# Kernel optimization log

Hardware: AMD Instinct MI355X
Metric: run time of the kernel (lower is better)

## Reference

```python
import jax, jax.numpy as jnp
import numpy as np

B, S, H = 4, 2048, 512
DEPTH, EXP = 2, 4
MAX_LR = 0.1
C = 8            # n_chunks
L = S // C       # chunk length
HE = H * EXP


def _l2norm(x, eps=1e-12):
    n = jnp.sqrt(jnp.sum(x * x, axis=-1, keepdims=True))
    return x / jnp.maximum(n, eps)


def _mem_fwd(mw1, mb1, mw2, mb2, x):
    # ResLinear: residual MLP blocks, x <- x + W2 @ silu(W1 @ x + b1) + b2
    for d in range(DEPTH):
        h = jax.nn.silu(x @ mw1[d].T + mb1[d])
        x = x + h @ mw2[d].T + mb2[d]
    return x


def setup_inputs() -> dict:
    key = jax.random.key(0)
    ks = jax.random.split(key, 9)
    s = 1.0 / np.sqrt(H)
    s2 = 1.0 / np.sqrt(HE)
    return {
        "x": jax.random.normal(ks[0], (B, S, H), jnp.float32),
        "wq": jax.random.normal(ks[1], (H, H), jnp.float32) * s, "bq": jnp.zeros((H,), jnp.float32),
        "wk": jax.random.normal(ks[2], (H, H), jnp.float32) * s, "bk": jnp.zeros((H,), jnp.float32),
        "wv": jax.random.normal(ks[3], (H, H), jnp.float32) * s, "bv": jnp.zeros((H,), jnp.float32),
        "wlr": jax.random.normal(ks[4], (1, H), jnp.float32) * s, "blr": jnp.zeros((1,), jnp.float32),
        "wf": jax.random.normal(ks[5], (1, H), jnp.float32) * s, "bf": jnp.zeros((1,), jnp.float32),
        "wm": jax.random.normal(ks[6], (1, H), jnp.float32) * s, "bm": jnp.zeros((1,), jnp.float32),
        "mw1": jax.random.normal(ks[7], (DEPTH, HE, H), jnp.float32) * s,
        "mb1": jnp.zeros((DEPTH, HE), jnp.float32),
        "mw2": jax.random.normal(ks[8], (DEPTH, H, HE), jnp.float32) * s2,
        "mb2": jnp.zeros((DEPTH, H), jnp.float32),
        "mom_w1": jnp.zeros((DEPTH, HE, H), jnp.float32),
        "mom_b1": jnp.zeros((DEPTH, HE), jnp.float32),
        "mom_w2": jnp.zeros((DEPTH, H, HE), jnp.float32),
        "mom_b2": jnp.zeros((DEPTH, H), jnp.float32),
    }


def reference(x, wq, bq, wk, bk, wv, bv, wlr, blr, wf, bf, wm, bm,
              mw1, mb1, mw2, mb2, mom_w1, mom_b1, mom_w2, mom_b2):
    # projections (non-generating path; S % C == 0 so no padding)
    q = _l2norm(x @ wq.T + bq)                            # [B,S,H]
    k = _l2norm(x @ wk.T + bk).reshape(B, C, L, H)
    v = (x @ wv.T + bv).reshape(B, C, L, H)
    lr = jax.nn.sigmoid(x @ wlr.T + blr).reshape(B, C, L, 1) * MAX_LR
    forget = jax.nn.sigmoid(x @ wf.T + bf).reshape(B, C, L, 1)
    momg = jax.nn.sigmoid(x @ wm.T + bm).reshape(B, C, L, 1)

    mem = (mw1, mb1, mw2, mb2)

    def chunk_loss(mem_params, k_c, v_c, lr_c):
        # k_c,v_c: [B,L,H]; lr_c: [B,L,1]
        preds = _mem_fwd(*mem_params, k_c)
        loss = jnp.mean((preds - v_c) ** 2, axis=-1)      # [B,L]
        return jnp.sum(loss * lr_c[..., 0])

    # per-chunk synthetic gradients of the memory MLP, then mean over chunks
    grads = jax.vmap(jax.grad(chunk_loss), in_axes=(None, 1, 1, 1))(mem, k, v, lr)
    grads = jax.tree_util.tree_map(lambda g: jnp.mean(g, axis=0), grads)

    alpha = jnp.mean(forget, axis=(1, 2, 3))              # [B] forget gate
    theta = jnp.mean(lr, axis=(1, 2, 3))                  # [B] adaptive lr
    eta = jnp.mean(momg, axis=(1, 2, 3))                  # [B] momentum gate

    def update(p, g, m):
        shp = (B,) + (1,) * p.ndim
        a, t, e = alpha.reshape(shp), theta.reshape(shp), eta.reshape(shp)
        m_b = e * m[None] - t * g[None]                   # [B,*p.shape]
        return jnp.mean(p[None] * (1.0 - a) + m_b, axis=0)

    moms = (mom_w1, mom_b1, mom_w2, mom_b2)
    new_mem = tuple(update(p, g, m) for p, g, m in zip(mem, grads, moms))

    return _mem_fwd(*new_mem, q)                          # [B,S,H]
```

## Files before the change

### kernel.cpp

```cpp
#include <hip/hip_runtime.h>
#include <cstdint>
#include <cstddef>


#define NROWS 8192
#define HDIM  512
#define HEDIM 2048
#define NCHUNK 8
#define BK    64
#define DPCOEF (2.0f / (HDIM * NCHUNK))

typedef unsigned short u16;
typedef __attribute__((ext_vector_type(8))) unsigned short u16x8;
typedef __attribute__((ext_vector_type(8))) short bf16x8;
typedef __attribute__((ext_vector_type(4))) float f32x4;

__device__ __forceinline__ float sigmoidf_(float x){ return 1.0f/(1.0f+__expf(-x)); }
__device__ __forceinline__ float siluf_(float x){ return x*sigmoidf_(x); }
__device__ __forceinline__ float dsiluf_(float x){ float s=sigmoidf_(x); return s*(1.0f+x*(1.0f-s)); }
__device__ __forceinline__ u16 bf1_(float x){
    union{float f; unsigned u;} v; v.f = x;
    return (u16)((v.u + 0x7fffu + ((v.u>>16)&1u)) >> 16);
}
__device__ __forceinline__ unsigned bfpack_(float a, float b){
    union{float f; unsigned u;} ua, ub; ua.f = a; ub.f = b;
    unsigned ra = (ua.u + 0x7fffu + ((ua.u>>16)&1u)) >> 16;
    unsigned rb = (ub.u + 0x7fffu + ((ub.u>>16)&1u)) & 0xffff0000u;
    return ra | rb;
}
__device__ __forceinline__ float bf2f_(u16 h){
    union{unsigned u; float f;} v; v.u = ((unsigned)h) << 16; return v.f;
}
__device__ __forceinline__ int swkey_(int row){
    return (((row>>3)&1)<<2) | (((row>>4)&1)<<1) | ((row>>5)&1);
}
__device__ __forceinline__ void gl_lds16(const u16* g, u16* l){
    __builtin_amdgcn_global_load_lds(
        (const __attribute__((address_space(1))) unsigned*)g,
        (__attribute__((address_space(3))) unsigned*)l, 16, 0, 0);
}

template<int MODE, bool ATR>
__global__ __launch_bounds__(256)
void mgemm_k(const u16* __restrict__ A, const u16* __restrict__ B,
             const float* __restrict__ bias, const float* __restrict__ resF,
             const u16* __restrict__ resB, const u16* __restrict__ aux,
             const float* __restrict__ vf, const float* __restrict__ lrs,
             float* __restrict__ outF, u16* __restrict__ outB, u16* __restrict__ outB2,
             int M, int N, int K, int lda, int ldb, int ldv)
{
    __shared__ __align__(128) u16 As[128*64];
    __shared__ __align__(128) u16 Bs[128*64];
    const int tid = threadIdx.x;
    const int lane = tid & 63, wvi = tid >> 6;
    const int wm = wvi >> 1, wn = wvi & 1;
    const int lr = lane & 15, lq = lane >> 4;

    const int gx = gridDim.x;
    const int nwg = gx * gridDim.y;
    int bid = blockIdx.y * gx + blockIdx.x;
    bid = (bid & 7) * (nwg >> 3) + (bid >> 3);
    const int m0 = (bid / gx) * 128, n0 = (bid % gx) * 128;

    int kbeg = 0, kend = K;
    if (MODE == 3){ const int ks = K >> 4; kbeg = blockIdx.z * ks; kend = kbeg + ks; }

    f32x4 acc[4][4];
    const f32x4 zz = {0.f,0.f,0.f,0.f};
    #pragma unroll
    for (int i = 0; i < 4; ++i)
        #pragma unroll
        for (int j = 0; j < 4; ++j) acc[i][j] = zz;

    for (int k0 = kbeg; k0 < kend; k0 += BK) {
        if (!ATR) {
            #pragma unroll
            for (int it = 0; it < 4; ++it){
                const int seg = it*4 + wvi;
                const int key = (((seg&1)<<2)|(((seg>>1)&1)<<1)|((seg>>2)&1));
                const int row = seg*8 + (lane>>3);
                const int chunk = (lane&7) ^ key;
                gl_lds16(A + (size_t)(m0+row)*lda + k0 + chunk*8, &As[seg*512]);
                gl_lds16(B + (size_t)(n0+row)*ldb + k0 + chunk*8, &Bs[seg*512]);
            }
        } else {
            const int mc = tid & 15, kp = tid >> 4;
            const int key = (((mc&1)<<2)|(((mc>>1)&1)<<1)|((mc>>2)&1));
            const int cs = ((kp >> 1) ^ key) * 8 + (kp & 1) * 4;
            {
                const u16* p = A + (size_t)(k0 + 4*kp) * lda + m0 + mc*8;
                u16x8 r0 = *(const u16x8*)p;
                u16x8 r1 = *(const u16x8*)(p + lda);
                u16x8 r2 = *(const u16x8*)(p + 2*lda);
                u16x8 r3 = *(const u16x8*)(p + 3*lda);
                #pragma unroll
                for (int j = 0; j < 8; ++j){
                    uint2 w;
                    w.x = (unsigned)r0[j] | ((unsigned)r1[j] << 16);
                    w.y = (unsigned)r2[j] | ((unsigned)r3[j] << 16);
                    *(uint2*)&As[(mc*8 + j)*64 + cs] = w;
                }
            }
            {
                const u16* p = B + (size_t)(k0 + 4*kp) * ldb + n0 + mc*8;
                u16x8 r0 = *(const u16x8*)p;
                u16x8 r1 = *(const u16x8*)(p + ldb);
                u16x8 r2 = *(const u16x8*)(p + 2*ldb);
                u16x8 r3 = *(const u16x8*)(p + 3*ldb);
                #pragma unroll
                for (int j = 0; j < 8; ++j){
                    uint2 w;
                    w.x = (unsigned)r0[j] | ((unsigned)r1[j] << 16);
                    w.y = (unsigned)r2[j] | ((unsigned)r3[j] << 16);
                    *(uint2*)&Bs[(mc*8 + j)*64 + cs] = w;
                }
            }
        }
        __syncthreads();
        #pragma unroll
        for (int ks = 0; ks < 2; ++ks) {
            bf16x8 afr[4], bfr[4];
            #pragma unroll
            for (int i = 0; i < 4; ++i){
                const int ra = wm*64 + i*16 + lr, rb = wn*64 + i*16 + lr;
                afr[i] = *(const bf16x8*)&As[ra*64 + (((ks*4 + lq) ^ swkey_(ra)) << 3)];
                bfr[i] = *(const bf16x8*)&Bs[rb*64 + (((ks*4 + lq) ^ swkey_(rb)) << 3)];
            }
            #pragma unroll
            for (int mi = 0; mi < 4; ++mi)
                #pragma unroll
                for (int ni = 0; ni < 4; ++ni)
                    acc[mi][ni] = __builtin_amdgcn_mfma_f32_16x16x32_bf16(afr[mi], bfr[ni], acc[mi][ni], 0, 0, 0);
        }
        __syncthreads();
    }

    if (MODE == 3){
        unsigned* P32 = (unsigned*)outB;
        const size_t zb = (size_t)blockIdx.z * ((size_t)M * N / 2);
        #pragma unroll
        for (int ni = 0; ni < 4; ++ni){
            const int col = n0 + wn*64 + ni*16 + lr;
            #pragma unroll
            for (int mi = 0; mi < 4; ++mi){
                const int pr = (m0 + wm*64 + mi*16 + lq*4) >> 1;
                P32[zb + (size_t)pr*N + col]     = bfpack_(acc[mi][ni][0], acc[mi][ni][1]);
                P32[zb + (size_t)(pr+1)*N + col] = bfpack_(acc[mi][ni][2], acc[mi][ni][3]);
            }
        }
        return;
    }

    #pragma unroll
    for (int ni = 0; ni < 4; ++ni){
        const int col = n0 + wn*64 + ni*16 + lr;
        float bv = 0.0f;
        if (MODE==0 || MODE==1 || MODE==2 || MODE==6 || MODE==7 || MODE==8 || MODE==9) bv = bias[col];
        #pragma unroll
        for (int mi = 0; mi < 4; ++mi){
            const int rbase = m0 + wm*64 + mi*16 + lq*4;
            #pragma unroll
            for (int v = 0; v < 4; ++v){
                const int row = rbase + v;
                const size_t idx = (size_t)row * N + col;
                const float o = acc[mi][ni][v];
                if (MODE == 0){ outF[idx] = o + bv; }
                else if (MODE == 1){
                    const float u = o + bv;
                    outB[idx]  = bf1_(siluf_(u));
                    outB2[idx] = bf1_(dsiluf_(u));
                }
                else if (MODE == 2){ outB[idx] = bf1_(siluf_(o + bv)); }
                else if (MODE == 4){ outB[idx] = bf1_(o * bf2f_(aux[idx])); }
                else if (MODE == 5){ outB[idx] = bf1_(o + resF[idx]); }
                else if (MODE == 6){ const float t = o + bv + resF[idx]; outF[idx] = t; outB[idx] = bf1_(t); }
                else if (MODE == 7){ outF[idx] = o + bv + resF[idx]; }
                else if (MODE == 8){
                    const float t = o + bv + bf2f_(resB[idx]);
                    const float g = lrs[row] * DPCOEF * (t - vf[(size_t)row * ldv + col]);
                    outF[idx] = g; outB[idx] = bf1_(g);
                }
                else if (MODE == 9){ outB[idx] = bf1_(o + bv + bf2f_(resB[idx])); }
            }
        }
    }
}

#define XSLOTS   (NROWS*HDIM/8)
#define W1SLOTS  (2*HEDIM*HDIM/8)
#define KVQSLOTS (3*HDIM*HDIM/8)
__global__ __launch_bounds__(256)
void prep_all_k(const float* __restrict__ x,  u16* __restrict__ xb,
                const float* __restrict__ mw1, u16* __restrict__ mw1b,
                const float* __restrict__ mw2, u16* __restrict__ mw2b,
                const float* __restrict__ wk, const float* __restrict__ wv,
                const float* __restrict__ wq, u16* __restrict__ wkvqb,
                const float* __restrict__ bk, const float* __restrict__ bv,
                const float* __restrict__ bq, float* __restrict__ bkvq)
{
    const int id = blockIdx.x * 256 + threadIdx.x;
    const int W1S = 2*HEDIM*HDIM/8;
    const float* src; u16* dst; int i;
    if (id < XSLOTS){ src = x; dst = xb; i = id; }
    else if (id < XSLOTS + W1S){ src = mw1; dst = mw1b; i = id - XSLOTS; }
    else if (id < XSLOTS + 2*W1S){ src = mw2; dst = mw2b; i = id - XSLOTS - W1S; }
    else if (id < XSLOTS + 2*W1S + KVQSLOTS){
        const int j = id - XSLOTS - 2*W1S;
        const int per = HDIM*HDIM/8;
        src = (j < per) ? wk : (j < 2*per ? wv : wq);
        i = (j < per) ? j : (j < 2*per ? j - per : j - 2*per);
        dst = wkvqb + (size_t)(j - i) * 8 * 0 + (size_t)j*8 - (size_t)i*8;
        dst = wkvqb + ((size_t)j - i) * 8;
    }
    else {
        const int j = id - XSLOTS - 2*W1S - KVQSLOTS;
        if (j < 3*HDIM)
            bkvq[j] = (j < HDIM) ? bk[j] : (j < 2*HDIM ? bv[j-HDIM] : bq[j-2*HDIM]);
        return;
    }
    const float4 a = *(const float4*)(src + (size_t)i*8);
    const float4 b = *(const float4*)(src + (size_t)i*8 + 4);
    u16x8 o;
    o[0]=bf1_(a.x); o[1]=bf1_(a.y); o[2]=bf1_(a.z); o[3]=bf1_(a.w);
    o[4]=bf1_(b.x); o[5]=bf1_(b.y); o[6]=bf1_(b.z); o[7]=bf1_(b.w);
    *(u16x8*)(dst + (size_t)i*8) = o;
}

__global__ __launch_bounds__(256)
void tcvt_k(const float* __restrict__ in, u16* __restrict__ out, int R, int C)
{
    __shared__ float t[32][33];
    const int tx = threadIdx.x & 31, ty = threadIdx.x >> 5;
    const int c0 = blockIdx.x * 32, r0 = blockIdx.y * 32;
    #pragma unroll
    for (int j = 0; j < 4; ++j)
        t[ty + 8*j][tx] = in[(size_t)(r0 + ty + 8*j) * C + c0 + tx];
    __syncthreads();
    #pragma unroll
    for (int j = 0; j < 4; ++j)
        out[(size_t)(c0 + ty + 8*j) * R + r0 + tx] = bf1_(t[tx][ty + 8*j]);
}

template<bool WF32>
__global__ __launch_bounds__(64)
void l2norm_k(const float* __restrict__ in, int ld,
              float* __restrict__ outF, u16* __restrict__ outB)
{
    const float* p = in + (size_t)blockIdx.x * ld;
    const int t = threadIdx.x;
    float4 v0 = *(const float4*)(p + t*8), v1 = *(const float4*)(p + t*8 + 4);
    float s = v0.x*v0.x+v0.y*v0.y+v0.z*v0.z+v0.w*v0.w
            + v1.x*v1.x+v1.y*v1.y+v1.z*v1.z+v1.w*v1.w;
    #pragma unroll
    for (int o = 1; o < 64; o <<= 1) s += __shfl_xor(s, o);
    const float sc = 1.0f / fmaxf(sqrtf(s), 1e-12f);
    v0.x*=sc; v0.y*=sc; v0.z*=sc; v0.w*=sc;
    v1.x*=sc; v1.y*=sc; v1.z*=sc; v1.w*=sc;
    if (WF32){
        float* q = outF + (size_t)blockIdx.x * HDIM;
        *(float4*)(q + t*8) = v0; *(float4*)(q + t*8 + 4) = v1;
    }
    u16x8 ob;
    ob[0]=bf1_(v0.x); ob[1]=bf1_(v0.y); ob[2]=bf1_(v0.z); ob[3]=bf1_(v0.w);
    ob[4]=bf1_(v1.x); ob[5]=bf1_(v1.y); ob[6]=bf1_(v1.z); ob[7]=bf1_(v1.w);
    *(u16x8*)(outB + (size_t)blockIdx.x * HDIM + t*8) = ob;
}

__global__ __launch_bounds__(64)
void gates_k(const float* __restrict__ x,
             const float* __restrict__ wlr, const float* __restrict__ blr,
             const float* __restrict__ wf,  const float* __restrict__ bfp,
             const float* __restrict__ wm,  const float* __restrict__ bm,
             float* __restrict__ lr_s, float* __restrict__ f_s, float* __restrict__ m_s)
{
    const size_t row = blockIdx.x;
    const float* p = x + row * HDIM;
    const int t = threadIdx.x;
    float s0 = 0.f, s1 = 0.f, s2 = 0.f;
    #pragma unroll
    for (int i = 0; i < 8; i += 4){
        float4 xv = *(const float4*)(p   + t*8 + i);
        float4 a  = *(const float4*)(wlr + t*8 + i);
        float4 b  = *(const float4*)(wf  + t*8 + i);
        float4 c  = *(const float4*)(wm  + t*8 + i);
        s0 += xv.x*a.x + xv.y*a.y + xv.z*a.z + xv.w*a.w;
        s1 += xv.x*b.x + xv.y*b.y + xv.z*b.z + xv.w*b.w;
        s2 += xv.x*c.x + xv.y*c.y + xv.z*c.z + xv.w*c.w;
    }
    #pragma unroll
    for (int o = 1; o < 64; o <<= 1){
        s0 += __shfl_xor(s0, o); s1 += __shfl_xor(s1, o); s2 += __shfl_xor(s2, o);
    }
    if (t == 0){
        lr_s[row] = sigmoidf_(s0 + blr[0]) * 0.1f;
        f_s[row]  = sigmoidf_(s1 + bfp[0]);
        m_s[row]  = sigmoidf_(s2 + bm[0]);
    }
}

__global__ __launch_bounds__(256)
void scalars_k(const float* __restrict__ lr_s, const float* __restrict__ f_s,
               const float* __restrict__ m_s, float* __restrict__ sc)
{
    __shared__ float sh0[256], sh1[256], sh2[256];
    const int t = threadIdx.x;
    float s0 = 0.f, s1 = 0.f, s2 = 0.f;
    for (int i = t; i < NROWS; i += 256){ s0 += f_s[i]; s1 += lr_s[i]; s2 += m_s[i]; }
    sh0[t] = s0; sh1[t] = s1; sh2[t] = s2;
    __syncthreads();
    for (int o = 128; o > 0; o >>= 1){
        if (t < o){ sh0[t] += sh0[t+o]; sh1[t] += sh1[t+o]; sh2[t] += sh2[t+o]; }
        __syncthreads();
    }
    if (t == 0){
        sc[0] = sh0[0] / (float)NROWS;
        sc[1] = sh1[0] / (float)NROWS;
        sc[2] = sh2[0] / (float)NROWS;
    }
}

template<typename T>
__global__ __launch_bounds__(64)
void colsum_part_k(const T* __restrict__ g, float* __restrict__ part, int cols)
{
    const int c = blockIdx.x * 64 + threadIdx.x;
    const int rc = blockIdx.y;
    const T* p = g + (size_t)rc * 128 * cols + c;
    float s = 0.f;
    for (int r = 0; r < 128; ++r){
        if (sizeof(T) == 2) s += bf2f_(*(const u16*)(p + (size_t)r * cols));
        else                s += *(const float*)(p + (size_t)r * cols);
    }
    part[(size_t)rc * cols + c] = s;
}

__global__ __launch_bounds__(256)
void colsum_upd_k(const float* __restrict__ part, const float* __restrict__ p,
                  const float* __restrict__ mom, const float* __restrict__ sc,
                  float* __restrict__ nb, int cols)
{
    const int c = blockIdx.x * 256 + threadIdx.x;
    if (c < cols){
        float s = 0.f;
        for (int r = 0; r < 64; ++r) s += part[(size_t)r * cols + c];
        nb[c] = p[c] * (1.0f - sc[0]) + sc[2] * mom[c] - sc[1] * s;
    }
}

__global__ __launch_bounds__(256)
void fupdate16p_k(const float* __restrict__ p, const unsigned* __restrict__ P32,
                  const float* __restrict__ mom, const float* __restrict__ sc,
                  u16* __restrict__ nWb, int N, int MN2)
{
    const int i = blockIdx.x * 256 + threadIdx.x;
    if (i < MN2){
        float g0 = 0.f, g1 = 0.f;
        #pragma unroll
        for (int z = 0; z < 16; ++z){
            const unsigned w = P32[(size_t)z * MN2 + i];
            g0 += bf2f_((u16)(w & 0xffffu));
            g1 += bf2f_((u16)(w >> 16));
        }
        const int c = i & (N - 1);
        const size_t r0 = ((size_t)(i / N) * 2) * N + c;
        nWb[r0]     = bf1_(p[r0]     * (1.0f - sc[0]) + sc[2] * mom[r0]     - sc[1] * g0);
        nWb[r0 + N] = bf1_(p[r0 + N] * (1.0f - sc[0]) + sc[2] * mom[r0 + N] - sc[1] * g1);
    }
}

extern "C" void kernel_launch(void* const* d_in, const int* in_sizes, int n_in,
                              void* d_out, int out_size, void* d_ws, size_t ws_size,
                              hipStream_t stream)
{
    const float* x      = (const float*)d_in[0];
    const float* wq     = (const float*)d_in[1];
    const float* bq     = (const float*)d_in[2];
    const float* wk     = (const float*)d_in[3];
    const float* bk     = (const float*)d_in[4];
    const float* wv     = (const float*)d_in[5];
    const float* bv     = (const float*)d_in[6];
    const float* wlr    = (const float*)d_in[7];
    const float* blr    = (const float*)d_in[8];
    const float* wf     = (const float*)d_in[9];
    const float* bfp    = (const float*)d_in[10];
    const float* wm     = (const float*)d_in[11];
    const float* bm     = (const float*)d_in[12];
    const float* mw1    = (const float*)d_in[13];
    const float* mb1    = (const float*)d_in[14];
    const float* mw2    = (const float*)d_in[15];
    const float* mb2    = (const float*)d_in[16];
    const float* mom_w1 = (const float*)d_in[17];
    const float* mom_b1 = (const float*)d_in[18];
    const float* mom_w2 = (const float*)d_in[19];
    const float* mom_b2 = (const float*)d_in[20];
    float* out = (float*)d_out;

    char* base = (char*)d_ws;
    size_t off = 0;
    auto alloc = [&](size_t bytes)->char*{ char* p = base + off; off += (bytes + 255) & ~(size_t)255; return p; };
    const size_t NHf  = (size_t)NROWS * HDIM  * 4;
    const size_t NHb  = (size_t)NROWS * HDIM  * 2;
    const size_t NHEb = (size_t)NROWS * HEDIM * 2;
    const int    WHALF = HEDIM * HDIM;

    float* F2   = (float*)alloc(NHf);
    u16*  xb    = (u16*) alloc(NHb);
    u16*  kb    = (u16*) alloc(NHb);
    u16*  x1b   = (u16*) alloc(NHb);
    u16*  g2b   = (u16*) alloc(NHb);
    u16*  hb    = (u16*) alloc(NHEb);
    u16*  db    = (u16*) alloc(NHEb);
    u16*  dhb   = (u16*) alloc(NHEb + NHf);
    u16*  wkvqb = (u16*) alloc((size_t)3*HDIM*HDIM*2);
    float* bkvq = (float*)alloc((size_t)3*HDIM*4);
    u16*  mw1b  = (u16*) alloc((size_t)2*WHALF*2);
    u16*  mw2b  = (u16*) alloc((size_t)2*WHALF*2);
    u16*  mw2Tb = (u16*) alloc((size_t)2*WHALF*2);
    u16*  mw1T1b= (u16*) alloc((size_t)WHALF*2);
    u16*  nW1b  = (u16*) alloc((size_t)2*WHALF*2);
    u16*  nW2b  = (u16*) alloc((size_t)2*WHALF*2);
    float* cpart= (float*)alloc((size_t)64*HEDIM*4);
    float* lr_s = (float*)alloc((size_t)NROWS*4);
    float* f_s  = (float*)alloc((size_t)NROWS*4);
    float* m_s  = (float*)alloc((size_t)NROWS*4);
    float* sc   = (float*)alloc(64);
    float* nb1  = (float*)alloc((size_t)2*HEDIM*4);
    float* nb2  = (float*)alloc((size_t)2*HDIM*4);
    u16* qb  = xb;
    u16* g1b = g2b;
    float* P3 = (float*)dhb;
    float* F1 = (float*)((char*)dhb + NHEb);
    unsigned* Pp = (unsigned*)db;

    const dim3 blk(256);
    const dim3 gKVQ (3*HDIM/128, NROWS/128);
    const dim3 gN512 (HDIM/128,  NROWS/128);
    const dim3 gN2048(HEDIM/128, NROWS/128);
    const dim3 gTN2  (HEDIM/128, HDIM/128, 16);
    const dim3 gTN1  (HDIM/128,  HEDIM/128, 16);
    const int MN2 = WHALF / 2;

    const float* mw1_1 = mw1 + (size_t)WHALF;
    const float* mw2_1 = mw2 + (size_t)WHALF;

    #define GARG(Ab,Bb,bi,rF,rB,ax,vv,ll,oF,oB,oB2,M,N,K,la,lb,lv) \
        ((const u16*)(Ab),(const u16*)(Bb),(const float*)(bi),(const float*)(rF),\
         (const u16*)(rB),(const u16*)(ax),(const float*)(vv),(const float*)(ll),\
         (float*)(oF),(u16*)(oB),(u16*)(oB2),(M),(N),(K),(la),(lb),(lv))

    {
        const int nblk = (XSLOTS + 2*(2*HEDIM*HDIM/8) + KVQSLOTS)/256 + (3*HDIM + 255)/256;
        prep_all_k<<<dim3(nblk), blk, 0, stream>>>(x, xb, mw1, mw1b, mw2, mw2b,
                                                   wk, wv, wq, wkvqb, bk, bv, bq, bkvq);
    }
    tcvt_k<<<dim3(HEDIM/32, HDIM/32), blk, 0, stream>>>(mw2,   mw2Tb,         HDIM, HEDIM);
    tcvt_k<<<dim3(HEDIM/32, HDIM/32), blk, 0, stream>>>(mw2_1, mw2Tb + WHALF, HDIM, HEDIM);
    tcvt_k<<<dim3(HDIM/32, HEDIM/32), blk, 0, stream>>>(mw1_1, mw1T1b,        HEDIM, HDIM);
    gates_k<<<NROWS, 64, 0, stream>>>(x, wlr, blr, wf, bfp, wm, bm, lr_s, f_s, m_s);
    scalars_k<<<1, blk, 0, stream>>>(lr_s, f_s, m_s, sc);

    mgemm_k<0,false><<<gKVQ, blk, 0, stream>>>GARG(xb, wkvqb, bkvq, 0,0,0,0,0, P3, 0,0, NROWS,3*HDIM,HDIM, HDIM,HDIM, 3*HDIM);
    l2norm_k<false><<<NROWS, 64, 0, stream>>>(P3,          3*HDIM, nullptr, kb);
    l2norm_k<true ><<<NROWS, 64, 0, stream>>>(P3 + 2*HDIM, 3*HDIM, F2, qb);

    mgemm_k<2,false><<<gN2048, blk, 0, stream>>>GARG(kb, mw1b, mb1, 0,0,0,0,0, 0, hb, 0, NROWS,HEDIM,HDIM, HDIM,HDIM, HEDIM);
    mgemm_k<9,false><<<gN512, blk, 0, stream>>>GARG(hb, mw2b, mb2, 0, kb, 0,0,0, 0, x1b, 0, NROWS,HDIM,HEDIM, HEDIM,HEDIM, HDIM);
    mgemm_k<1,false><<<gN2048, blk, 0, stream>>>GARG(x1b, mw1b+WHALF, mb1+HEDIM, 0,0,0,0,0, 0, hb, db, NROWS,HEDIM,HDIM, HDIM,HDIM, HEDIM);
    mgemm_k<8,false><<<gN512, blk, 0, stream>>>GARG(hb, mw2b+WHALF, mb2+HDIM, 0, x1b, 0, P3 + HDIM, lr_s, out, g2b, 0, NROWS,HDIM,HEDIM, HEDIM,HEDIM, 3*HDIM);

    colsum_part_k<float><<<dim3(HDIM/64,64), 64, 0, stream>>>(out, cpart, HDIM);
    colsum_upd_k<<<dim3(HDIM/256), blk, 0, stream>>>(cpart, mb2+HDIM, mom_b2+HDIM, sc, nb2+HDIM, HDIM);
    mgemm_k<4,false><<<gN2048, blk, 0, stream>>>GARG(g2b, mw2Tb+WHALF, 0,0,0, db, 0,0, 0, dhb, 0, NROWS,HEDIM,HDIM, HDIM,HDIM, HEDIM);
    mgemm_k<3,true><<<gTN2, blk, 0, stream>>>GARG(g2b, hb, 0,0,0,0,0,0, 0, Pp, 0, HDIM,HEDIM,NROWS, HDIM,HEDIM, HEDIM);
    fupdate16p_k<<<dim3((MN2+255)/256), blk, 0, stream>>>(mw2_1, Pp, mom_w2+WHALF, sc, nW2b+WHALF, HEDIM, MN2);
    colsum_part_k<u16><<<dim3(HEDIM/64,64), 64, 0, stream>>>(dhb, cpart, HEDIM);
    colsum_upd_k<<<dim3(HEDIM/256), blk, 0, stream>>>(cpart, mb1+HEDIM, mom_b1+HEDIM, sc, nb1+HEDIM, HEDIM);
    mgemm_k<3,true><<<gTN1, blk, 0, stream>>>GARG(dhb, x1b, 0,0,0,0,0,0, 0, Pp, 0, HEDIM,HDIM,NROWS, HEDIM,HDIM, HDIM);
    fupdate16p_k<<<dim3((MN2+255)/256), blk, 0, stream>>>(mw1_1, Pp, mom_w1+WHALF, sc, nW1b+WHALF, HDIM, MN2);
    mgemm_k<5,false><<<gN512, blk, 0, stream>>>GARG(dhb, mw1T1b, 0, out, 0,0,0,0, 0, g1b, 0, NROWS,HDIM,HEDIM, HEDIM,HEDIM, HDIM);

    colsum_part_k<u16><<<dim3(HDIM/64,64), 64, 0, stream>>>(g1b, cpart, HDIM);
    colsum_upd_k<<<dim3(HDIM/256), blk, 0, stream>>>(cpart, mb2, mom_b2, sc, nb2, HDIM);
    mgemm_k<1,false><<<gN2048, blk, 0, stream>>>GARG(kb, mw1b, mb1, 0,0,0,0,0, 0, hb, db, NROWS,HEDIM,HDIM, HDIM,HDIM, HEDIM);
    mgemm_k<4,false><<<gN2048, blk, 0, stream>>>GARG(g1b, mw2Tb, 0,0,0, db, 0,0, 0, dhb, 0, NROWS,HEDIM,HDIM, HDIM,HDIM, HEDIM);
    mgemm_k<3,true><<<gTN2, blk, 0, stream>>>GARG(g1b, hb, 0,0,0,0,0,0, 0, Pp, 0, HDIM,HEDIM,NROWS, HDIM,HEDIM, HEDIM);
    fupdate16p_k<<<dim3((MN2+255)/256), blk, 0, stream>>>(mw2, Pp, mom_w2, sc, nW2b, HEDIM, MN2);
    colsum_part_k<u16><<<dim3(HEDIM/64,64), 64, 0, stream>>>(dhb, cpart, HEDIM);
    colsum_upd_k<<<dim3(HEDIM/256), blk, 0, stream>>>(cpart, mb1, mom_b1, sc, nb1, HEDIM);
    mgemm_k<3,true><<<gTN1, blk, 0, stream>>>GARG(dhb, kb, 0,0,0,0,0,0, 0, Pp, 0, HEDIM,HDIM,NROWS, HEDIM,HDIM, HDIM);
    fupdate16p_k<<<dim3((MN2+255)/256), blk, 0, stream>>>(mw1, Pp, mom_w1, sc, nW1b, HDIM, MN2);

    mgemm_k<2,false><<<gN2048, blk, 0, stream>>>GARG(qb, nW1b, nb1, 0,0,0,0,0, 0, hb, 0, NROWS,HEDIM,HDIM, HDIM,HDIM, HEDIM);
    mgemm_k<6,false><<<gN512, blk, 0, stream>>>GARG(hb, nW2b, nb2, F2, 0,0,0,0, F1, x1b, 0, NROWS,HDIM,HEDIM, HEDIM,HEDIM, HDIM);
    mgemm_k<2,false><<<gN2048, blk, 0, stream>>>GARG(x1b, nW1b+WHALF, nb1+HEDIM, 0,0,0,0,0, 0, hb, 0, NROWS,HEDIM,HDIM, HDIM,HDIM, HEDIM);
    mgemm_k<7,false><<<gN512, blk, 0, stream>>>GARG(hb, nW2b+WHALF, nb2+HDIM, F1, 0,0,0,0, out, 0,0, NROWS,HDIM,HEDIM, HEDIM,HEDIM, HDIM);

    #undef GARG
    (void)in_sizes; (void)n_in; (void)out_size; (void)ws_size;
}
```

Baseline: 807.4 us.

## Double-buffer GEMM K-loop and keep layer-0 activations to skip recompute

The NT GEMM path now stages the next K tile into a second LDS buffer via global_load_lds while the current tile runs MFMA, with explicit vmcnt waits and raw barriers in place of __syncthreads. The TN path prefetches the next tile into registers and writes it to LDS after the current MFMA step. Separately, when the workspace is large enough, the first-layer hidden activation and its silu derivative are saved during the forward pass, so the backward pass no longer recomputes the layer-0 GEMM. This doubles LDS use for NT kernels, which may lower occupancy, and uses more workspace memory.

```diff
diff --git a/kernel.cpp b/kernel.cpp
--- a/kernel.cpp
+++ b/kernel.cpp
@@ -39,6 +39,10 @@
         (const __attribute__((address_space(1))) unsigned*)g,
         (__attribute__((address_space(3))) unsigned*)l, 16, 0, 0);
 }
+__device__ __forceinline__ void bar_(){ asm volatile("s_barrier" ::: "memory"); }
+#define VMCNT8  asm volatile("s_waitcnt vmcnt(8)" ::: "memory")
+#define VMCNT0  asm volatile("s_waitcnt vmcnt(0)" ::: "memory")
+#define LGKM0   asm volatile("s_waitcnt lgkmcnt(0)" ::: "memory")
 
 template<int MODE, bool ATR>
 __global__ __launch_bounds__(256)
@@ -49,8 +53,9 @@
              float* __restrict__ outF, u16* __restrict__ outB, u16* __restrict__ outB2,
              int M, int N, int K, int lda, int ldb, int ldv)
 {
-    __shared__ __align__(128) u16 As[128*64];
-    __shared__ __align__(128) u16 Bs[128*64];
+    constexpr int NBUF = ATR ? 1 : 2;
+    __shared__ __align__(128) u16 As[NBUF][128*64];
+    __shared__ __align__(128) u16 Bs[NBUF][128*64];
     const int tid = threadIdx.x;
     const int lane = tid & 63, wvi = tid >> 6;
     const int wm = wvi >> 1, wn = wvi & 1;
@@ -64,6 +69,7 @@
 
     int kbeg = 0, kend = K;
     if (MODE == 3){ const int ks = K >> 4; kbeg = blockIdx.z * ks; kend = kbeg + ks; }
+    const int nk = (kend - kbeg) / BK;
 
     f32x4 acc[4][4];
     const f32x4 zz = {0.f,0.f,0.f,0.f};
@@ -72,59 +78,52 @@
         #pragma unroll
         for (int j = 0; j < 4; ++j) acc[i][j] = zz;
 
-    for (int k0 = kbeg; k0 < kend; k0 += BK) {
-        if (!ATR) {
-            #pragma unroll
-            for (int it = 0; it < 4; ++it){
-                const int seg = it*4 + wvi;
-                const int key = (((seg&1)<<2)|(((seg>>1)&1)<<1)|((seg>>2)&1));
-                const int row = seg*8 + (lane>>3);
-                const int chunk = (lane&7) ^ key;
-                gl_lds16(A + (size_t)(m0+row)*lda + k0 + chunk*8, &As[seg*512]);
-                gl_lds16(B + (size_t)(n0+row)*ldb + k0 + chunk*8, &Bs[seg*512]);
-            }
-        } else {
-            const int mc = tid & 15, kp = tid >> 4;
-            const int key = (((mc&1)<<2)|(((mc>>1)&1)<<1)|((mc>>2)&1));
-            const int cs = ((kp >> 1) ^ key) * 8 + (kp & 1) * 4;
-            {
-                const u16* p = A + (size_t)(k0 + 4*kp) * lda + m0 + mc*8;
-                u16x8 r0 = *(const u16x8*)p;
-                u16x8 r1 = *(const u16x8*)(p + lda);
-                u16x8 r2 = *(const u16x8*)(p + 2*lda);
-                u16x8 r3 = *(const u16x8*)(p + 3*lda);
-                #pragma unroll
-                for (int j = 0; j < 8; ++j){
-                    uint2 w;
-                    w.x = (unsigned)r0[j] | ((unsigned)r1[j] << 16);
-                    w.y = (unsigned)r2[j] | ((unsigned)r3[j] << 16);
-                    *(uint2*)&As[(mc*8 + j)*64 + cs] = w;
-                }
-            }
-            {
-                const u16* p = B + (size_t)(k0 + 4*kp) * ldb + n0 + mc*8;
-                u16x8 r0 = *(const u16x8*)p;
-                u16x8 r1 = *(const u16x8*)(p + ldb);
-                u16x8 r2 = *(const u16x8*)(p + 2*ldb);
-                u16x8 r3 = *(const u16x8*)(p + 3*ldb);
-                #pragma unroll
-                for (int j = 0; j < 8; ++j){
-                    uint2 w;
-                    w.x = (unsigned)r0[j] | ((unsigned)r1[j] << 16);
-                    w.y = (unsigned)r2[j] | ((unsigned)r3[j] << 16);
-                    *(uint2*)&Bs[(mc*8 + j)*64 + cs] = w;
-                }
-            }
-        }
-        __syncthreads();
+    const int mc = tid & 15, kp = tid >> 4;
+    const int tkey = (((mc&1)<<2)|(((mc>>1)&1)<<1)|((mc>>2)&1));
+    const int tcs = ((kp >> 1) ^ tkey) * 8 + (kp & 1) * 4;
+    u16x8 rgA0, rgA1, rgA2, rgA3, rgB0, rgB1, rgB2, rgB3;
+
+    auto stageNT = [&](int k0, int b){
+        #pragma unroll
+        for (int it = 0; it < 4; ++it){
+            const int seg = it*4 + wvi;
+            const int key = (((seg&1)<<2)|(((seg>>1)&1)<<1)|((seg>>2)&1));
+            const int row = seg*8 + (lane>>3);
+            const int chunk = (lane&7) ^ key;
+            gl_lds16(A + (size_t)(m0+row)*lda + k0 + chunk*8, &As[b][seg*512]);
+            gl_lds16(B + (size_t)(n0+row)*ldb + k0 + chunk*8, &Bs[b][seg*512]);
+        }
+    };
+    auto gloadTN = [&](int k0){
+        const u16* pa = A + (size_t)(k0 + 4*kp) * lda + m0 + mc*8;
+        rgA0 = *(const u16x8*)pa;          rgA1 = *(const u16x8*)(pa + lda);
+        rgA2 = *(const u16x8*)(pa+2*lda);  rgA3 = *(const u16x8*)(pa + 3*lda);
+        const u16* pb = B + (size_t)(k0 + 4*kp) * ldb + n0 + mc*8;
+        rgB0 = *(const u16x8*)pb;          rgB1 = *(const u16x8*)(pb + ldb);
+        rgB2 = *(const u16x8*)(pb+2*ldb);  rgB3 = *(const u16x8*)(pb + 3*ldb);
+    };
+    auto dswriteTN = [&](){
+        #pragma unroll
+        for (int j = 0; j < 8; ++j){
+            uint2 w;
+            w.x = (unsigned)rgA0[j] | ((unsigned)rgA1[j] << 16);
+            w.y = (unsigned)rgA2[j] | ((unsigned)rgA3[j] << 16);
+            *(uint2*)&As[0][(mc*8 + j)*64 + tcs] = w;
+            uint2 v;
+            v.x = (unsigned)rgB0[j] | ((unsigned)rgB1[j] << 16);
+            v.y = (unsigned)rgB2[j] | ((unsigned)rgB3[j] << 16);
+            *(uint2*)&Bs[0][(mc*8 + j)*64 + tcs] = v;
+        }
+    };
+    auto mfmaStep = [&](int b){
         #pragma unroll
         for (int ks = 0; ks < 2; ++ks) {
             bf16x8 afr[4], bfr[4];
             #pragma unroll
             for (int i = 0; i < 4; ++i){
                 const int ra = wm*64 + i*16 + lr, rb = wn*64 + i*16 + lr;
-                afr[i] = *(const bf16x8*)&As[ra*64 + (((ks*4 + lq) ^ swkey_(ra)) << 3)];
-                bfr[i] = *(const bf16x8*)&Bs[rb*64 + (((ks*4 + lq) ^ swkey_(rb)) << 3)];
+                afr[i] = *(const bf16x8*)&As[b][ra*64 + (((ks*4 + lq) ^ swkey_(ra)) << 3)];
+                bfr[i] = *(const bf16x8*)&Bs[b][rb*64 + (((ks*4 + lq) ^ swkey_(rb)) << 3)];
             }
             #pragma unroll
             for (int mi = 0; mi < 4; ++mi)
@@ -132,7 +131,33 @@
                 for (int ni = 0; ni < 4; ++ni)
                     acc[mi][ni] = __builtin_amdgcn_mfma_f32_16x16x32_bf16(afr[mi], bfr[ni], acc[mi][ni], 0, 0, 0);
         }
-        __syncthreads();
+    };
+
+    if (!ATR) {
+        stageNT(kbeg, 0);
+        int cur = 0;
+        for (int i = 0; i < nk; ++i){
+            const int k0 = kbeg + i*BK;
+            if (i + 1 < nk){ stageNT(k0 + BK, cur ^ 1); VMCNT8; }
+            else           { VMCNT0; }
+            bar_();
+            mfmaStep(cur);
+            bar_();
+            cur ^= 1;
+        }
+    } else {
+        gloadTN(kbeg);
+        dswriteTN();
+        LGKM0; bar_();
+        for (int i = 0; i < nk; ++i){
+            const int k0 = kbeg + i*BK;
+            const bool hn = (i + 1 < nk);
+            if (hn) gloadTN(k0 + BK);
+            mfmaStep(0);
+            bar_();
+            if (hn){ dswriteTN(); LGKM0; }
+            bar_();
+        }
     }
 
     if (MODE == 3){
@@ -187,7 +212,6 @@
 }
 
 #define XSLOTS   (NROWS*HDIM/8)
-#define W1SLOTS  (2*HEDIM*HDIM/8)
 #define KVQSLOTS (3*HDIM*HDIM/8)
 __global__ __launch_bounds__(256)
 void prep_all_k(const float* __restrict__ x,  u16* __restrict__ xb,
@@ -209,8 +233,7 @@
         const int per = HDIM*HDIM/8;
         src = (j < per) ? wk : (j < 2*per ? wv : wq);
         i = (j < per) ? j : (j < 2*per ? j - per : j - 2*per);
-        dst = wkvqb + (size_t)(j - i) * 8 * 0 + (size_t)j*8 - (size_t)i*8;
-        dst = wkvqb + ((size_t)j - i) * 8;
+        dst = wkvqb + ((size_t)(j - i)) * 8;
     }
     else {
         const int j = id - XSLOTS - 2*W1S - KVQSLOTS;
@@ -426,6 +449,11 @@
     float* sc   = (float*)alloc(64);
     float* nb1  = (float*)alloc((size_t)2*HEDIM*4);
     float* nb2  = (float*)alloc((size_t)2*HDIM*4);
+
+    const bool keep0 = (ws_size >= off + 2*NHEb + 1024);
+    u16* h0b = keep0 ? (u16*)alloc(NHEb) : hb;
+    u16* d0b = keep0 ? (u16*)alloc(NHEb) : db;
+
     u16* qb  = xb;
     u16* g1b = g2b;
     float* P3 = (float*)dhb;
@@ -463,8 +491,11 @@
     l2norm_k<false><<<NROWS, 64, 0, stream>>>(P3,          3*HDIM, nullptr, kb);
     l2norm_k<true ><<<NROWS, 64, 0, stream>>>(P3 + 2*HDIM, 3*HDIM, F2, qb);
 
-    mgemm_k<2,false><<<gN2048, blk, 0, stream>>>GARG(kb, mw1b, mb1, 0,0,0,0,0, 0, hb, 0, NROWS,HEDIM,HDIM, HDIM,HDIM, HEDIM);
-    mgemm_k<9,false><<<gN512, blk, 0, stream>>>GARG(hb, mw2b, mb2, 0, kb, 0,0,0, 0, x1b, 0, NROWS,HDIM,HEDIM, HEDIM,HEDIM, HDIM);
+    if (keep0)
+        mgemm_k<1,false><<<gN2048, blk, 0, stream>>>GARG(kb, mw1b, mb1, 0,0,0,0,0, 0, h0b, d0b, NROWS,HEDIM,HDIM, HDIM,HDIM, HEDIM);
+    else
+        mgemm_k<2,false><<<gN2048, blk, 0, stream>>>GARG(kb, mw1b, mb1, 0,0,0,0,0, 0, hb, 0, NROWS,HEDIM,HDIM, HDIM,HDIM, HEDIM);
+    mgemm_k<9,false><<<gN512, blk, 0, stream>>>GARG(h0b, mw2b, mb2, 0, kb, 0,0,0, 0, x1b, 0, NROWS,HDIM,HEDIM, HEDIM,HEDIM, HDIM);
     mgemm_k<1,false><<<gN2048, blk, 0, stream>>>GARG(x1b, mw1b+WHALF, mb1+HEDIM, 0,0,0,0,0, 0, hb, db, NROWS,HEDIM,HDIM, HDIM,HDIM, HEDIM);
     mgemm_k<8,false><<<gN512, blk, 0, stream>>>GARG(hb, mw2b+WHALF, mb2+HDIM, 0, x1b, 0, P3 + HDIM, lr_s, out, g2b, 0, NROWS,HDIM,HEDIM, HEDIM,HEDIM, 3*HDIM);
 
@@ -481,9 +512,10 @@
 
     colsum_part_k<u16><<<dim3(HDIM/64,64), 64, 0, stream>>>(g1b, cpart, HDIM);
     colsum_upd_k<<<dim3(HDIM/256), blk, 0, stream>>>(cpart, mb2, mom_b2, sc, nb2, HDIM);
-    mgemm_k<1,false><<<gN2048, blk, 0, stream>>>GARG(kb, mw1b, mb1, 0,0,0,0,0, 0, hb, db, NROWS,HEDIM,HDIM, HDIM,HDIM, HEDIM);
-    mgemm_k<4,false><<<gN2048, blk, 0, stream>>>GARG(g1b, mw2Tb, 0,0,0, db, 0,0, 0, dhb, 0, NROWS,HEDIM,HDIM, HDIM,HDIM, HEDIM);
-    mgemm_k<3,true><<<gTN2, blk, 0, stream>>>GARG(g1b, hb, 0,0,0,0,0,0, 0, Pp, 0, HDIM,HEDIM,NROWS, HDIM,HEDIM, HEDIM);
+    if (!keep0)
+        mgemm_k<1,false><<<gN2048, blk, 0, stream>>>GARG(kb, mw1b, mb1, 0,0,0,0,0, 0, hb, db, NROWS,HEDIM,HDIM, HDIM,HDIM, HEDIM);
+    mgemm_k<4,false><<<gN2048, blk, 0, stream>>>GARG(g1b, mw2Tb, 0,0,0, d0b, 0,0, 0, dhb, 0, NROWS,HEDIM,HDIM, HDIM,HDIM, HEDIM);
+    mgemm_k<3,true><<<gTN2, blk, 0, stream>>>GARG(g1b, h0b, 0,0,0,0,0,0, 0, Pp, 0, HDIM,HEDIM,NROWS, HDIM,HEDIM, HEDIM);
     fupdate16p_k<<<dim3((MN2+255)/256), blk, 0, stream>>>(mw2, Pp, mom_w2, sc, nW2b, HEDIM, MN2);
     colsum_part_k<u16><<<dim3(HEDIM/64,64), 64, 0, stream>>>(dhb, cpart, HEDIM);
     colsum_upd_k<<<dim3(HEDIM/256), blk, 0, stream>>>(cpart, mb1, mom_b1, sc, nb1, HEDIM);
@@ -496,5 +528,5 @@
     mgemm_k<7,false><<<gN512, blk, 0, stream>>>GARG(hb, nW2b+WHALF, nb2+HDIM, F1, 0,0,0,0, out, 0,0, NROWS,HDIM,HEDIM, HEDIM,HEDIM, HDIM);
 
     #undef GARG
-    (void)in_sizes; (void)n_in; (void)out_size; (void)ws_size;
-}
+    (void)in_sizes; (void)n_in; (void)out_size;
+}
```

After: 790.4 us. 2.1% less time.
